# Performance work log

Measured on AMD Instinct MI355X. Metric: run time of the kernel, lower is better.

The kernel has to match this reference:

```python
import jax, jax.numpy as jnp
import numpy as np

B, SQ, SK = 2, 2048, 2048
D_MODEL, N_HEADS = 1024, 16
D_HEAD = D_MODEL // N_HEADS
LN_EPS = 1e-5


def _ln(x, w, b):
    # per-head LayerNorm over last dim (d_head)
    mu = jnp.mean(x, axis=-1, keepdims=True)
    var = jnp.mean(jnp.square(x - mu), axis=-1, keepdims=True)
    return (x - mu) * jax.lax.rsqrt(var + LN_EPS) * w + b


def setup_inputs() -> dict:
    key = jax.random.key(0)
    ks = jax.random.split(key, 8)
    sd = 1.0 / np.sqrt(D_MODEL)
    so = 1.0 / np.sqrt(D_HEAD)
    return {
        "x_q": jax.random.normal(ks[0], (B, SQ, D_MODEL), jnp.float32),
        "x_kv": jax.random.normal(ks[1], (B, SK, D_MODEL), jnp.float32),
        "mask": jnp.tril(jnp.ones((SQ, SK), dtype=bool)),  # causal
        "W_Q": jax.random.normal(ks[2], (N_HEADS, D_MODEL, D_HEAD), jnp.float32) * sd,
        "W_K": jax.random.normal(ks[3], (N_HEADS, D_MODEL, D_HEAD), jnp.float32) * sd,
        "W_V": jax.random.normal(ks[4], (N_HEADS, D_MODEL, D_HEAD), jnp.float32) * sd,
        "W_O": jax.random.normal(ks[5], (N_HEADS, D_HEAD, D_MODEL), jnp.float32) * so,
        "b_Q": jnp.zeros((N_HEADS, D_HEAD), jnp.float32),
        "b_K": jnp.zeros((N_HEADS, D_HEAD), jnp.float32),
        "b_V": jnp.zeros((N_HEADS, D_HEAD), jnp.float32),
        "b_O": jnp.zeros((D_MODEL,), jnp.float32),
        "ln1_w": jnp.ones((D_HEAD,), jnp.float32),
        "ln1_b": jnp.zeros((D_HEAD,), jnp.float32),
        "ln2_w": jnp.ones((D_HEAD,), jnp.float32),
        "ln2_b": jnp.zeros((D_HEAD,), jnp.float32),
    }


def reference(x_q, x_kv, mask, W_Q, W_K, W_V, W_O, b_Q, b_K, b_V, b_O,
              ln1_w, ln1_b, ln2_w, ln2_b):
    # QKV projections: b s d, n d h -> b s n h
    q = jnp.einsum('bsd,ndh->bsnh', x_q, W_Q) + b_Q
    k = jnp.einsum('bsd,ndh->bsnh', x_kv, W_K) + b_K
    v = jnp.einsum('bsd,ndh->bsnh', x_kv, W_V) + b_V
    # QK-norm (ln_first=False, rope=None -> just apply LN after projections)
    q = _ln(q, ln1_w, ln1_b)
    k = _ln(k, ln2_w, ln2_b)
    # NOTE: no 1/sqrt(d_head) scaling, matching the original module
    att = jnp.einsum('bqnh,bknh->bnqk', q, k)
    att = jnp.where(mask, att, -jnp.inf)
    probas = jax.nn.softmax(att, axis=-1)
    z = jnp.einsum('bnqk,bknh->bqnh', probas, v)
    out = jnp.einsum('bqnh,nhd->bqd', z, W_O) + b_O
    return (out, k, v)
```

## Files before the change

kernel.cpp:

```cpp
#include <hip/hip_runtime.h>
#include <hip/hip_bf16.h>

#define B_   2
#define SQ_  2048
#define DM_  1024
#define NH_  16
#define DH_  64

typedef __attribute__((ext_vector_type(8))) short          bf16x8;
typedef __attribute__((ext_vector_type(4))) short          bf16x4;
typedef __attribute__((ext_vector_type(8))) unsigned short u16x8;
typedef __attribute__((ext_vector_type(4))) float          f32x4;

__device__ __forceinline__ unsigned short f2bf(float f) {
    union { __hip_bfloat16 h; unsigned short u; } c;
    c.h = __float2bfloat16(f);
    return c.u;
}
__device__ __forceinline__ float gsum16(float v) {
    v += __shfl_xor(v, 1);
    v += __shfl_xor(v, 2);
    v += __shfl_xor(v, 4);
    v += __shfl_xor(v, 8);
    return v;
}

__device__ __forceinline__ f32x4 mfma16(bf16x4 a, bf16x4 b, f32x4 c) {
#if __has_builtin(__builtin_amdgcn_mfma_f32_16x16x16bf16_1k)
    return __builtin_amdgcn_mfma_f32_16x16x16bf16_1k(a, b, c, 0, 0, 0);
#else
    asm("v_mfma_f32_16x16x16_bf16 %0, %1, %2, %0" : "+v"(c) : "v"(a), "v"(b));
    return c;
#endif
}

__device__ __forceinline__ void gll16(const unsigned short* g, unsigned short* l) {
    __builtin_amdgcn_global_load_lds(
        (const __attribute__((address_space(1))) unsigned int*)g,
        (__attribute__((address_space(3))) unsigned int*)l,
        16, 0, 0);
}

__global__ __launch_bounds__(256) void prep_all(
    const float* __restrict__ W_Q, const float* __restrict__ W_K,
    const float* __restrict__ W_V, const float* __restrict__ W_O,
    const float* __restrict__ x_q, const float* __restrict__ x_kv,
    unsigned short* __restrict__ WTq, unsigned short* __restrict__ WTkv,
    unsigned short* __restrict__ WTo,
    unsigned short* __restrict__ xqbf, unsigned short* __restrict__ xkvbf)
{
    const int bid = blockIdx.x, tid = threadIdx.x;
    if (bid >= 1024) {
        const int cid = bid - 1024;
        const float* src = (cid < 512) ? x_q : x_kv;
        unsigned short* dst = (cid < 512) ? xqbf : xkvbf;
        const size_t base = (size_t)(cid & 511) * 8192 + tid * 4;
#pragma unroll
        for (int i = 0; i < 8; ++i) {
            const float4 v = *(const float4*)(src + base + i * 1024);
            ushort4 o;
            o.x = f2bf(v.x); o.y = f2bf(v.y); o.z = f2bf(v.z); o.w = f2bf(v.w);
            *(ushort4*)(dst + base + i * 1024) = o;
        }
        return;
    }
    __shared__ float t[64][65];
    const float* src; unsigned short* dst; int R, C, r0, c0;
    if (bid < 768) {
        const int which = bid >> 8, rem = bid & 255;
        const int rblk = rem & 15, zz = rem >> 4;
        src = (which == 0) ? W_Q : (which == 1) ? W_K : W_V;
        dst = (which == 0) ? WTq : (which == 1) ? WTkv : (WTkv + (1u << 20));
        src += (size_t)65536 * zz;
        dst += (size_t)65536 * zz;
        R = 1024; C = 64; r0 = rblk * 64; c0 = 0;
    } else {
        const int rem = bid - 768;
        src = W_O; dst = WTo; R = 1024; C = 1024;
        r0 = (rem & 15) * 64; c0 = (rem >> 4) * 64;
    }
    const int lr = tid >> 6, lc = tid & 63;
#pragma unroll
    for (int i = 0; i < 16; ++i)
        t[lr + i * 4][lc] = src[(size_t)(r0 + lr + i * 4) * C + c0 + lc];
    __syncthreads();
    const int u = tid & 15, w0 = tid >> 4;
#pragma unroll
    for (int i = 0; i < 4; ++i) {
        const int cl = w0 + i * 16;
        ushort4 o;
        o.x = f2bf(t[4 * u + 0][cl]);
        o.y = f2bf(t[4 * u + 1][cl]);
        o.z = f2bf(t[4 * u + 2][cl]);
        o.w = f2bf(t[4 * u + 3][cl]);
        *(ushort4*)&dst[(size_t)(c0 + cl) * R + r0 + 4 * u] = o;
    }
}

template <int TM, int MODE, int NT>
__device__ __forceinline__ void gemm_body(
    unsigned short (*__restrict__ As)[64], unsigned short (*__restrict__ Bs)[64],
    int bx, int by, const unsigned short* __restrict__ Abf,
    const unsigned short* __restrict__ WT,
    const float* __restrict__ biasK, const float* __restrict__ biasV,
    const float* __restrict__ lnw, const float* __restrict__ lnb,
    float* __restrict__ Cf, float* __restrict__ Cf2,
    unsigned short* __restrict__ Cb, unsigned short* __restrict__ CbT, int tid)
{
    constexpr int NW    = NT / 64;
    constexpr int WROWS = 2 * TM / NW;
    constexpr int MI    = WROWS / 16;
    constexpr int RP    = NT / 8;
    constexpr int APASS = TM / RP;
    constexpr int BPASS = 128 / RP;

    const int m0 = by * TM;
    const int c0 = bx * 128;

    const int wid = tid >> 6, lane = tid & 63;
    const int wm = (wid >> 1) * WROWS;
    const int wn = (wid & 1) * 64;
    const int l15 = lane & 15, qd = lane >> 4;

    const int srow  = tid >> 3;
    const int pslot = tid & 7;
    const int sslot = pslot ^ (srow & 7);
    const unsigned short* Ag = Abf + (size_t)(m0 + srow) * 1024 + sslot * 8;
    const unsigned short* Bg = WT  + (size_t)(c0 + srow) * 1024 + sslot * 8;
    unsigned short* Al = &As[srow][pslot * 8];
    unsigned short* Bl = &Bs[srow][pslot * 8];

    const f32x4 zero4 = {0.f, 0.f, 0.f, 0.f};
    f32x4 acc[MI][4];
#pragma unroll
    for (int mi = 0; mi < MI; ++mi)
#pragma unroll
        for (int ni = 0; ni < 4; ++ni) acc[mi][ni] = zero4;

    const int r7 = l15 & 7;

    for (int kb = 0; kb < 16; ++kb) {
        const size_t kof = (size_t)kb * 64;
        __syncthreads();
#pragma unroll
        for (int j = 0; j < APASS; ++j)
            gll16(Ag + (size_t)j * RP * 1024 + kof, Al + j * RP * 64);
#pragma unroll
        for (int j = 0; j < BPASS; ++j)
            gll16(Bg + (size_t)j * RP * 1024 + kof, Bl + j * RP * 64);
        __syncthreads();
#pragma unroll
        for (int ks = 0; ks < 2; ++ks) {
            const int cs = ((ks * 4 + qd) ^ r7) * 8;
            bf16x8 af[MI], bfr[4];
#pragma unroll
            for (int mi = 0; mi < MI; ++mi)
                af[mi] = *(const bf16x8*)&As[wm + mi * 16 + l15][cs];
#pragma unroll
            for (int ni = 0; ni < 4; ++ni)
                bfr[ni] = *(const bf16x8*)&Bs[wn + ni * 16 + l15][cs];
#pragma unroll
            for (int mi = 0; mi < MI; ++mi)
#pragma unroll
                for (int ni = 0; ni < 4; ++ni)
                    acc[mi][ni] = __builtin_amdgcn_mfma_f32_16x16x32_bf16(
                        af[mi], bfr[ni], acc[mi][ni], 0, 0, 0);
        }
    }

    const float* bias = (MODE == 1 && c0 >= 1024) ? biasV : biasK;
    float bv[4];
#pragma unroll
    for (int ni = 0; ni < 4; ++ni) bv[ni] = bias[(c0 + wn + ni * 16 + l15) & 1023];
#pragma unroll
    for (int mi = 0; mi < MI; ++mi)
#pragma unroll
        for (int ni = 0; ni < 4; ++ni)
#pragma unroll
            for (int r = 0; r < 4; ++r) acc[mi][ni][r] += bv[ni];

    if constexpr (MODE != 2) {
        const bool doLN = (MODE == 0) || (c0 < 1024);
        if (doLN) {
            float w4[4], lb4[4];
#pragma unroll
            for (int ni = 0; ni < 4; ++ni) {
                w4[ni]  = lnw[ni * 16 + l15];
                lb4[ni] = lnb[ni * 16 + l15];
            }
#pragma unroll
            for (int mi = 0; mi < MI; ++mi)
#pragma unroll
                for (int r = 0; r < 4; ++r) {
                    float s1 = acc[mi][0][r] + acc[mi][1][r] + acc[mi][2][r] + acc[mi][3][r];
                    const float mu = gsum16(s1) * (1.0f / 64.0f);
                    float s2 = acc[mi][0][r] * acc[mi][0][r] + acc[mi][1][r] * acc[mi][1][r]
                             + acc[mi][2][r] * acc[mi][2][r] + acc[mi][3][r] * acc[mi][3][r];
                    const float var = gsum16(s2) * (1.0f / 64.0f) - mu * mu;
                    const float rstd = rsqrtf(var + 1e-5f);
#pragma unroll
                    for (int ni = 0; ni < 4; ++ni)
                        acc[mi][ni][r] = (acc[mi][ni][r] - mu) * rstd * w4[ni] + lb4[ni];
                }
        }
    }

    if constexpr (MODE == 0) {
#pragma unroll
        for (int mi = 0; mi < MI; ++mi)
#pragma unroll
            for (int r = 0; r < 4; ++r) {
                const size_t grow = m0 + wm + mi * 16 + qd * 4 + r;
#pragma unroll
                for (int ni = 0; ni < 4; ++ni)
                    Cb[grow * 1024 + c0 + wn + ni * 16 + l15] = f2bf(acc[mi][ni][r]);
            }
    } else if constexpr (MODE == 2) {
#pragma unroll
        for (int mi = 0; mi < MI; ++mi)
#pragma unroll
            for (int r = 0; r < 4; ++r) {
                const size_t grow = m0 + wm + mi * 16 + qd * 4 + r;
#pragma unroll
                for (int ni = 0; ni < 4; ++ni)
                    Cf[grow * 1024 + c0 + wn + ni * 16 + l15] = acc[mi][ni][r];
            }
    } else {
        if (c0 < 1024) {
#pragma unroll
            for (int mi = 0; mi < MI; ++mi)
#pragma unroll
                for (int r = 0; r < 4; ++r) {
                    const size_t grow = m0 + wm + mi * 16 + qd * 4 + r;
#pragma unroll
                    for (int ni = 0; ni < 4; ++ni) {
                        const int gcol = c0 + wn + ni * 16 + l15;
                        Cf[grow * 1024 + gcol] = acc[mi][ni][r];
                        Cb[grow * 1024 + gcol] = f2bf(acc[mi][ni][r]);
                    }
                }
        } else {
#pragma unroll
            for (int mi = 0; mi < MI; ++mi) {
                const int growb = m0 + wm + mi * 16 + qd * 4;
                const int bb_ = growb >> 11, ss = growb & 2047;
#pragma unroll
                for (int ni = 0; ni < 4; ++ni) {
                    const int gv = c0 - 1024 + wn + ni * 16 + l15;
                    const int hh = gv >> 6, dd = gv & 63;
#pragma unroll
                    for (int r = 0; r < 4; ++r)
                        Cf2[(size_t)(growb + r) * 1024 + gv] = acc[mi][ni][r];
                    ushort4 w;
                    w.x = f2bf(acc[mi][ni][0]); w.y = f2bf(acc[mi][ni][1]);
                    w.z = f2bf(acc[mi][ni][2]); w.w = f2bf(acc[mi][ni][3]);
                    *(ushort4*)&CbT[(((size_t)bb_ * NH_ + hh) * DH_ + dd) * SQ_ + ss] = w;
                }
            }
        }
    }
}

__global__ __launch_bounds__(512) void qkv_fused(
    const unsigned short* __restrict__ xqbf, const unsigned short* __restrict__ xkvbf,
    const unsigned short* __restrict__ WTq, const unsigned short* __restrict__ WTkv,
    const float* __restrict__ b_Q, const float* __restrict__ b_K,
    const float* __restrict__ b_V,
    const float* __restrict__ ln1w, const float* __restrict__ ln1b,
    const float* __restrict__ ln2w, const float* __restrict__ ln2b,
    float* __restrict__ kout, float* __restrict__ vout,
    unsigned short* __restrict__ qz, unsigned short* __restrict__ kbf,
    unsigned short* __restrict__ vbfT)
{
    __shared__ __align__(16) unsigned short As[128][64];
    __shared__ __align__(16) unsigned short Bs[128][64];
    const int bid = blockIdx.x, tid = threadIdx.x;
    if (bid < 512) {
        gemm_body<128, 1, 512>(As, Bs, bid & 15, bid >> 4, xkvbf, WTkv, b_K, b_V,
                               ln2w, ln2b, kout, vout, kbf, vbfT, tid);
    } else {
        const int b2 = bid - 512;
        gemm_body<128, 0, 512>(As, Bs, b2 & 7, b2 >> 3, xqbf, WTq, b_Q, nullptr,
                               ln1w, ln1b, nullptr, nullptr, qz, nullptr, tid);
    }
}

__global__ __launch_bounds__(512) void o_gemm(
    const unsigned short* __restrict__ zbf, const unsigned short* __restrict__ WTo,
    const float* __restrict__ b_O, float* __restrict__ out)
{
    __shared__ __align__(16) unsigned short As[64][64];
    __shared__ __align__(16) unsigned short Bs[128][64];
    gemm_body<64, 2, 512>(As, Bs, blockIdx.x, blockIdx.y, zbf, WTo, b_O, nullptr,
                          nullptr, nullptr, out, nullptr, nullptr, nullptr,
                          threadIdx.x);
}

__global__ __launch_bounds__(512) void attn_mfma(
    unsigned short* __restrict__ qz, const unsigned short* __restrict__ kbf,
    const unsigned short* __restrict__ vbfT)
{
    __shared__ __align__(16) unsigned short Ks[2][128][72];
    __shared__ __align__(16) unsigned short VsT[2][64][136];

    const int tid = threadIdx.x;
    const int h = blockIdx.y, b = blockIdx.z;
    const int wid = tid >> 6, lane = tid & 63;
    const int g = wid & 3, p = wid >> 2;
    const int l15 = lane & 15, qd = lane >> 4;
    const int srow = tid >> 2, scol = (tid & 3) * 16;
    const int vrow = tid >> 3, vcol = (tid & 7) * 16;

    const size_t kbase = (size_t)b * SQ_ * DM_ + (size_t)h * DH_;
    const size_t vbase = ((size_t)b * NH_ + h) * DH_ * (size_t)SQ_;
    const f32x4 zero4 = {0.f, 0.f, 0.f, 0.f};
    const float LOG2E = 1.44269504f, MBIAS = 46.1662413f;

    float* zs = (float*)&Ks[0][0][0];
    float* ls = (float*)&VsT[0][0][0];

    for (int pass = 0; pass < 2; ++pass) {
        const int qt = pass ? blockIdx.x : 31 - blockIdx.x;

        bf16x8 qf[2];
        {
            const unsigned short* qp =
                qz + kbase + (size_t)(qt * 64 + g * 16 + l15) * DM_ + qd * 8;
            qf[0] = *(const bf16x8*)(qp);
            qf[1] = *(const bf16x8*)(qp + 32);
        }

        f32x4 z[4];
#pragma unroll
        for (int ni = 0; ni < 4; ++ni) z[ni] = zero4;
        float l_i = 0.f;

        {
            const unsigned short* ks = kbf + kbase + (size_t)srow * DM_ + scol;
            const u16x8 a0 = *(const u16x8*)(ks);
            const u16x8 a1 = *(const u16x8*)(ks + 8);
            const unsigned short* vs = vbfT + vbase + (size_t)vrow * SQ_ + vcol;
            const u16x8 b0 = *(const u16x8*)(vs);
            const u16x8 b1 = *(const u16x8*)(vs + 8);
            *(u16x8*)&Ks[0][srow][scol + 0]  = a0;
            *(u16x8*)&Ks[0][srow][scol + 8]  = a1;
            *(u16x8*)&VsT[0][vrow][vcol + 0] = b0;
            *(u16x8*)&VsT[0][vrow][vcol + 8] = b1;
        }
        __syncthreads();

        const int NS = (qt >> 1) + 1;
        for (int st = 0; st < NS; ++st) {
            const int cur = st & 1;

            u16x8 kr0, kr1, vr0, vr1;
            if (st < NS - 1) {
                const unsigned short* ks =
                    kbf + kbase + (size_t)((st + 1) * 128 + srow) * DM_ + scol;
                kr0 = *(const u16x8*)(ks);
                kr1 = *(const u16x8*)(ks + 8);
                const unsigned short* vs =
                    vbfT + vbase + (size_t)vrow * SQ_ + (st + 1) * 128 + vcol;
                vr0 = *(const u16x8*)(vs);
                vr1 = *(const u16x8*)(vs + 8);
            }

            const int kt = st * 2 + p;
            if (kt <= qt) {
                f32x4 s[4];
#pragma unroll
                for (int mi = 0; mi < 4; ++mi) s[mi] = zero4;
#pragma unroll
                for (int ks2 = 0; ks2 < 2; ++ks2)
#pragma unroll
                    for (int mi = 0; mi < 4; ++mi) {
                        const bf16x8 af = *(const bf16x8*)
                            &Ks[cur][p * 64 + mi * 16 + l15][ks2 * 32 + qd * 8];
                        s[mi] = __builtin_amdgcn_mfma_f32_16x16x32_bf16(
                            af, qf[ks2], s[mi], 0, 0, 0);
                    }

                if (kt == qt) {
#pragma unroll
                    for (int mi = 0; mi < 4; ++mi)
#pragma unroll
                        for (int r = 0; r < 4; ++r)
                            if (mi * 16 + qd * 4 + r > g * 16 + l15)
                                s[mi][r] = -3.0e38f;
                }

                float ts[4];
                bf16x4 pa[4];
#pragma unroll
                for (int mi = 0; mi < 4; ++mi) {
#pragma unroll
                    for (int r = 0; r < 4; ++r)
                        s[mi][r] = __builtin_amdgcn_exp2f(
                            fmaf(s[mi][r], LOG2E, -MBIAS));
                    ts[mi] = (s[mi][0] + s[mi][1]) + (s[mi][2] + s[mi][3]);
                    pa[mi][0] = (short)f2bf(s[mi][0]);
                    pa[mi][1] = (short)f2bf(s[mi][1]);
                    pa[mi][2] = (short)f2bf(s[mi][2]);
                    pa[mi][3] = (short)f2bf(s[mi][3]);
                }
                float rs = (ts[0] + ts[1]) + (ts[2] + ts[3]);
                rs += __shfl_xor(rs, 16);
                rs += __shfl_xor(rs, 32);
                l_i += rs;

#pragma unroll
                for (int mi = 0; mi < 4; ++mi)
#pragma unroll
                    for (int ni = 0; ni < 4; ++ni) {
                        const bf16x4 bv = *(const bf16x4*)
                            &VsT[cur][ni * 16 + l15][p * 64 + mi * 16 + qd * 4];
                        z[ni] = mfma16(pa[mi], bv, z[ni]);
                    }
            }

            if (st < NS - 1) {
                *(u16x8*)&Ks[cur ^ 1][srow][scol + 0]  = kr0;
                *(u16x8*)&Ks[cur ^ 1][srow][scol + 8]  = kr1;
                *(u16x8*)&VsT[cur ^ 1][vrow][vcol + 0] = vr0;
                *(u16x8*)&VsT[cur ^ 1][vrow][vcol + 8] = vr1;
            }
            __syncthreads();
        }

        if (p == 1) {
#pragma unroll
            for (int ni = 0; ni < 4; ++ni)
                *(f32x4*)&zs[((g * 4 + ni) * 64 + lane) * 4] = z[ni];
            ls[g * 64 + lane] = l_i;
        }
        __syncthreads();
        if (p == 0) {
            const float l_tot = l_i + ls[g * 64 + lane];
#pragma unroll
            for (int ni = 0; ni < 4; ++ni) {
                const f32x4 zo = *(const f32x4*)&zs[((g * 4 + ni) * 64 + lane) * 4];
#pragma unroll
                for (int r = 0; r < 4; ++r) z[ni][r] += zo[r];
            }
            const float linv = 1.0f / l_tot;
#pragma unroll
            for (int r = 0; r < 4; ++r) {
                const float lr_ = __shfl(linv, qd * 4 + r);
                const size_t row = (size_t)qt * 64 + g * 16 + qd * 4 + r;
#pragma unroll
                for (int ni = 0; ni < 4; ++ni)
                    qz[kbase + row * DM_ + ni * 16 + l15] = f2bf(z[ni][r] * lr_);
            }
        }
        __syncthreads();
    }
}

extern "C" void kernel_launch(void* const* d_in, const int* in_sizes, int n_in,
                              void* d_out, int out_size, void* d_ws, size_t ws_size,
                              hipStream_t stream)
{
    const float* x_q  = (const float*)d_in[0];
    const float* x_kv = (const float*)d_in[1];
    const float* W_Q  = (const float*)d_in[3];
    const float* W_K  = (const float*)d_in[4];
    const float* W_V  = (const float*)d_in[5];
    const float* W_O  = (const float*)d_in[6];
    const float* b_Q  = (const float*)d_in[7];
    const float* b_K  = (const float*)d_in[8];
    const float* b_V  = (const float*)d_in[9];
    const float* b_O  = (const float*)d_in[10];
    const float* ln1w = (const float*)d_in[11];
    const float* ln1b = (const float*)d_in[12];
    const float* ln2w = (const float*)d_in[13];
    const float* ln2b = (const float*)d_in[14];

    const size_t NTOK = (size_t)B_ * SQ_;
    float* out  = (float*)d_out;
    float* kout = out + NTOK * DM_;
    float* vout = kout + NTOK * DM_;

    unsigned short* xqbf  = (unsigned short*)out;
    unsigned short* xkvbf = xqbf + (1u << 22);

    unsigned short* wsu  = (unsigned short*)d_ws;
    unsigned short* WTq  = wsu;
    unsigned short* WTkv = WTq + (1u << 20);
    unsigned short* WTo  = WTkv + (2u << 20);
    unsigned short* qz   = WTo + (1u << 20);
    unsigned short* kbf  = qz + (1u << 22);
    unsigned short* vbfT = kbf + (1u << 22);

    prep_all<<<2048, 256, 0, stream>>>(W_Q, W_K, W_V, W_O, x_q, x_kv,
                                       WTq, WTkv, WTo, xqbf, xkvbf);

    qkv_fused<<<768, 512, 0, stream>>>(xqbf, xkvbf, WTq, WTkv, b_Q, b_K, b_V,
                                       ln1w, ln1b, ln2w, ln2b,
                                       kout, vout, qz, kbf, vbfT);

    attn_mfma<<<dim3(16, NH_, B_), 512, 0, stream>>>(qz, kbf, vbfT);

    o_gemm<<<dim3(8, 64), 512, 0, stream>>>(qz, WTo, b_O, out);
}
```

Baseline: 229.7 us.

## Double-buffer GEMM LDS tiles with async prefetch and shrink QKV M-tile

```diff
diff --git a/kernel.cpp b/kernel.cpp
--- a/kernel.cpp
+++ b/kernel.cpp
@@ -32,6 +32,14 @@
     asm("v_mfma_f32_16x16x16_bf16 %0, %1, %2, %0" : "+v"(c) : "v"(a), "v"(b));
     return c;
 #endif
+}
+
+template <int N> __device__ __forceinline__ void waitv() {
+    if constexpr (N == 0)      asm volatile("s_waitcnt vmcnt(0)" ::: "memory");
+    else if constexpr (N == 2) asm volatile("s_waitcnt vmcnt(2)" ::: "memory");
+    else if constexpr (N == 3) asm volatile("s_waitcnt vmcnt(3)" ::: "memory");
+    else if constexpr (N == 4) asm volatile("s_waitcnt vmcnt(4)" ::: "memory");
+    else if constexpr (N == 6) asm volatile("s_waitcnt vmcnt(6)" ::: "memory");
 }
 
 __device__ __forceinline__ void gll16(const unsigned short* g, unsigned short* l) {
@@ -99,7 +107,8 @@
 
 template <int TM, int MODE, int NT>
 __device__ __forceinline__ void gemm_body(
-    unsigned short (*__restrict__ As)[64], unsigned short (*__restrict__ Bs)[64],
+    unsigned short* __restrict__ As,
+    unsigned short* __restrict__ Bs,
     int bx, int by, const unsigned short* __restrict__ Abf,
     const unsigned short* __restrict__ WT,
     const float* __restrict__ biasK, const float* __restrict__ biasV,
@@ -113,6 +122,7 @@
     constexpr int RP    = NT / 8;
     constexpr int APASS = TM / RP;
     constexpr int BPASS = 128 / RP;
+    constexpr int LOADS = APASS + BPASS;
 
     const int m0 = by * TM;
     const int c0 = bx * 128;
@@ -127,8 +137,8 @@
     const int sslot = pslot ^ (srow & 7);
     const unsigned short* Ag = Abf + (size_t)(m0 + srow) * 1024 + sslot * 8;
     const unsigned short* Bg = WT  + (size_t)(c0 + srow) * 1024 + sslot * 8;
-    unsigned short* Al = &As[srow][pslot * 8];
-    unsigned short* Bl = &Bs[srow][pslot * 8];
+    unsigned short* Al = As + srow * 64 + pslot * 8;
+    unsigned short* Bl = Bs + srow * 64 + pslot * 8;
 
     const f32x4 zero4 = {0.f, 0.f, 0.f, 0.f};
     f32x4 acc[MI][4];
@@ -139,26 +149,43 @@
 
     const int r7 = l15 & 7;
 
+#define STAGE(kb_, bi_)                                                        \
+    {                                                                          \
+        const size_t kof_ = (size_t)(kb_) * 64;                                \
+        _Pragma("unroll")                                                      \
+        for (int j = 0; j < APASS; ++j)                                        \
+            gll16(Ag + (size_t)j * RP * 1024 + kof_,                           \
+                  Al + (bi_) * (TM * 64) + j * RP * 64);                       \
+        _Pragma("unroll")                                                      \
+        for (int j = 0; j < BPASS; ++j)                                        \
+            gll16(Bg + (size_t)j * RP * 1024 + kof_,                           \
+                  Bl + (bi_) * (128 * 64) + j * RP * 64);                      \
+    }
+
+    STAGE(0, 0)
     for (int kb = 0; kb < 16; ++kb) {
-        const size_t kof = (size_t)kb * 64;
-        __syncthreads();
-#pragma unroll
-        for (int j = 0; j < APASS; ++j)
-            gll16(Ag + (size_t)j * RP * 1024 + kof, Al + j * RP * 64);
-#pragma unroll
-        for (int j = 0; j < BPASS; ++j)
-            gll16(Bg + (size_t)j * RP * 1024 + kof, Bl + j * RP * 64);
-        __syncthreads();
+        const int cur = kb & 1;
+        if (kb < 15) {
+            STAGE(kb + 1, cur ^ 1)
+            waitv<LOADS>();
+        } else {
+            waitv<0>();
+        }
+        __builtin_amdgcn_sched_barrier(0);
+        __builtin_amdgcn_s_barrier();
+        __builtin_amdgcn_sched_barrier(0);
 #pragma unroll
         for (int ks = 0; ks < 2; ++ks) {
             const int cs = ((ks * 4 + qd) ^ r7) * 8;
             bf16x8 af[MI], bfr[4];
 #pragma unroll
             for (int mi = 0; mi < MI; ++mi)
-                af[mi] = *(const bf16x8*)&As[wm + mi * 16 + l15][cs];
+                af[mi] = *(const bf16x8*)(As + cur * (TM * 64) +
+                                          (wm + mi * 16 + l15) * 64 + cs);
 #pragma unroll
             for (int ni = 0; ni < 4; ++ni)
-                bfr[ni] = *(const bf16x8*)&Bs[wn + ni * 16 + l15][cs];
+                bfr[ni] = *(const bf16x8*)(Bs + cur * (128 * 64) +
+                                           (wn + ni * 16 + l15) * 64 + cs);
 #pragma unroll
             for (int mi = 0; mi < MI; ++mi)
 #pragma unroll
@@ -166,7 +193,10 @@
                     acc[mi][ni] = __builtin_amdgcn_mfma_f32_16x16x32_bf16(
                         af[mi], bfr[ni], acc[mi][ni], 0, 0, 0);
         }
-    }
+        __builtin_amdgcn_sched_barrier(0);
+        __builtin_amdgcn_s_barrier();
+    }
+#undef STAGE
 
     const float* bias = (MODE == 1 && c0 >= 1024) ? biasV : biasK;
     float bv[4];
@@ -272,16 +302,16 @@
     unsigned short* __restrict__ qz, unsigned short* __restrict__ kbf,
     unsigned short* __restrict__ vbfT)
 {
-    __shared__ __align__(16) unsigned short As[128][64];
-    __shared__ __align__(16) unsigned short Bs[128][64];
+    __shared__ __align__(16) unsigned short As[2 * 64 * 64];
+    __shared__ __align__(16) unsigned short Bs[2 * 128 * 64];
     const int bid = blockIdx.x, tid = threadIdx.x;
-    if (bid < 512) {
-        gemm_body<128, 1, 512>(As, Bs, bid & 15, bid >> 4, xkvbf, WTkv, b_K, b_V,
-                               ln2w, ln2b, kout, vout, kbf, vbfT, tid);
+    if (bid < 1024) {
+        gemm_body<64, 1, 512>(As, Bs, bid & 15, bid >> 4, xkvbf, WTkv, b_K, b_V,
+                              ln2w, ln2b, kout, vout, kbf, vbfT, tid);
     } else {
-        const int b2 = bid - 512;
-        gemm_body<128, 0, 512>(As, Bs, b2 & 7, b2 >> 3, xqbf, WTq, b_Q, nullptr,
-                               ln1w, ln1b, nullptr, nullptr, qz, nullptr, tid);
+        const int b2 = bid - 1024;
+        gemm_body<64, 0, 512>(As, Bs, b2 & 7, b2 >> 3, xqbf, WTq, b_Q, nullptr,
+                              ln1w, ln1b, nullptr, nullptr, qz, nullptr, tid);
     }
 }
 
@@ -289,8 +319,8 @@
     const unsigned short* __restrict__ zbf, const unsigned short* __restrict__ WTo,
     const float* __restrict__ b_O, float* __restrict__ out)
 {
-    __shared__ __align__(16) unsigned short As[64][64];
-    __shared__ __align__(16) unsigned short Bs[128][64];
+    __shared__ __align__(16) unsigned short As[2 * 64 * 64];
+    __shared__ __align__(16) unsigned short Bs[2 * 128 * 64];
     gemm_body<64, 2, 512>(As, Bs, blockIdx.x, blockIdx.y, zbf, WTo, b_O, nullptr,
                           nullptr, nullptr, out, nullptr, nullptr, nullptr,
                           threadIdx.x);
@@ -494,9 +524,9 @@
     prep_all<<<2048, 256, 0, stream>>>(W_Q, W_K, W_V, W_O, x_q, x_kv,
                                        WTq, WTkv, WTo, xqbf, xkvbf);
 
-    qkv_fused<<<768, 512, 0, stream>>>(xqbf, xkvbf, WTq, WTkv, b_Q, b_K, b_V,
-                                       ln1w, ln1b, ln2w, ln2b,
-                                       kout, vout, qz, kbf, vbfT);
+    qkv_fused<<<1536, 512, 0, stream>>>(xqbf, xkvbf, WTq, WTkv, b_Q, b_K, b_V,
+                                        ln1w, ln1b, ln2w, ln2b,
+                                        kout, vout, qz, kbf, vbfT);
 
     attn_mfma<<<dim3(16, NH_, B_), 512, 0, stream>>>(qz, kbf, vbfT);
 
```

After: 225.9 us. No clear change (-1.7%).
